# Kernel optimization log

Measured on AMD Instinct MI355X. Metric: run time of the kernel, lower is better.

## Reference

```python
import jax, jax.numpy as jnp
import numpy as np

IN_CH = 256
HID = 64
HEADS = 3 * 0 + 4  # num_heads


def setup_inputs() -> dict:
    key = jax.random.key(0)
    ks = jax.random.split(key, 5)
    B, C, H, W = 2, IN_CH, 64, 64
    x = jax.random.normal(ks[0], (B, C, H, W), dtype=jnp.float32)
    # per-head embed conv (kernel 1 -> stored as [heads, 3*HID, C]); kaiming fan_out-ish scale
    w_embed = jax.random.normal(ks[1], (HEADS, 3 * HID, C), dtype=jnp.float32) * np.float32(np.sqrt(2.0 / (3 * HID)))
    b_embed = jnp.zeros((HEADS, 3 * HID), dtype=jnp.float32)
    # output ConvTranspose2d(hidden*heads -> C, kernel 1): weight [hidden*heads, C]
    w_out = jax.random.normal(ks[2], (HEADS * HID, C), dtype=jnp.float32) * np.float32(np.sqrt(2.0 / C))
    b_out = jnp.zeros((C,), dtype=jnp.float32)
    return {"x": x, "w_embed": w_embed, "b_embed": b_embed, "w_out": w_out, "b_out": b_out}


def reference(x, w_embed, b_embed, w_out, b_out):
    B, C, H, W = x.shape
    N = H * W
    nH = w_embed.shape[0]
    D = w_embed.shape[1] // 3
    scale = D ** -0.5
    # 1x1 embed conv per head: [B, nH, 3D, N]
    xf = x.reshape(B, C, N)
    qkv = jnp.einsum('bcn,hdc->bhdn', xf, w_embed) + b_embed[None, :, :, None]
    q, k, v = jnp.split(qkv, 3, axis=2)  # each [B, nH, D, N]
    attn = jnp.einsum('bhci,bhcj->bhij', q, k) * scale  # [B, nH, N, N]
    attn = jax.nn.softmax(attn, axis=-1)
    y = jnp.einsum('bhij,bhcj->bhci', attn, v)  # [B, nH, D, N]
    y = y.reshape(B, nH * D, N)
    # output 1x1 transposed conv (kernel 1 == plain 1x1 projection)
    out = jnp.einsum('bkn,kc->bcn', y, w_out) + b_out[None, :, None]
    out = out.reshape(B, C, H, W)
    return out + x  # residual
```

## Files before the change

kernel.cpp:

```cpp
#include <hip/hip_runtime.h>
#include <hip/hip_bf16.h>

#define NH   4
#define D_   64
#define N_   4096
#define C_   256
#define ME   768
#define QSCALE 0.18033688f

typedef float    f32x4  __attribute__((ext_vector_type(4)));
typedef float    f32x16 __attribute__((ext_vector_type(16)));
typedef _Float16 f16x8  __attribute__((ext_vector_type(8)));
typedef _Float16 f16x4  __attribute__((ext_vector_type(4)));

__global__ __launch_bounds__(256) void prep_kernel(const float* __restrict__ x,
                                                   const float* __restrict__ w_out,
                                                   _Float16* __restrict__ xT,
                                                   _Float16* __restrict__ w_outT) {
    __shared__ float T[64][68];
    const int t = threadIdx.x, bx = blockIdx.x;
    if (bx < 512) {
        const int n0 = (bx & 63) * 64, c0 = ((bx >> 6) & 3) * 64, b = bx >> 8;
        const float* xp = x + ((size_t)b * C_ + c0) * N_ + n0;
        #pragma unroll
        for (int r = 0; r < 4; ++r) {
            int idx = r * 256 + t;
            int c = idx >> 4, ng = (idx & 15) * 4;
            *(f32x4*)&T[c][ng] = *(const f32x4*)(xp + (size_t)c * N_ + ng);
        }
        __syncthreads();
        _Float16* dp = xT + ((size_t)b * N_ + n0) * C_ + c0;
        #pragma unroll
        for (int r = 0; r < 2; ++r) {
            int idx = r * 256 + t;
            int n = idx >> 3, cg = (idx & 7) * 8;
            f16x8 v;
            #pragma unroll
            for (int j = 0; j < 8; ++j) v[j] = (_Float16)T[cg + j][n];
            *(f16x8*)(dp + (size_t)n * C_ + cg) = v;
        }
    } else {
        int tile = bx - 512;
        int tc = tile & 3, tk = tile >> 2;
        #pragma unroll
        for (int r = 0; r < 4; ++r) {
            int idx = r * 256 + t;
            int kl = idx >> 4, cl = (idx & 15) * 4;
            *(f32x4*)&T[kl][cl] = *(const f32x4*)(w_out + (size_t)(tk * 64 + kl) * C_ + tc * 64 + cl);
        }
        __syncthreads();
        #pragma unroll
        for (int r = 0; r < 2; ++r) {
            int idx = r * 256 + t;
            int cl = idx >> 3, kg = (idx & 7) * 8;
            f16x8 v;
            #pragma unroll
            for (int j = 0; j < 8; ++j) v[j] = (_Float16)T[kg + j][cl];
            *(f16x8*)(w_outT + (size_t)(tc * 64 + cl) * C_ + tk * 64 + kg) = v;
        }
    }
}

__global__ __launch_bounds__(256) void qkv_gemm(const _Float16* __restrict__ xT,
                                                const float* __restrict__ w_embed,
                                                const float* __restrict__ b_embed,
                                                _Float16* __restrict__ qT,
                                                _Float16* __restrict__ kT,
                                                _Float16* __restrict__ vB) {
    __shared__ __align__(16) union SM {
        struct { _Float16 A[64][40], X[64][40]; } s;
        float Os[64][68];
    } sm;
    const int n0 = blockIdx.x * 64, mt = blockIdx.y, b = blockIdx.z;
    const int m0 = mt * 64;
    const int t = threadIdx.x;
    const int lane = t & 63, w = t >> 6, quad = lane >> 4, l16 = lane & 15;
    const int srow = t >> 2, skoff = (t & 3) * 8;
    const int h = mt / 3, r3 = mt - h * 3;
    const float oscale = (r3 == 0) ? QSCALE : 1.0f;
    const float* ap = w_embed + (size_t)(m0 + srow) * C_ + skoff;
    const _Float16* xp = xT + ((size_t)b * N_ + n0 + srow) * C_ + skoff;
    f32x4 a0pre = *(const f32x4*)(ap);
    f32x4 a1pre = *(const f32x4*)(ap + 4);
    f16x8 xpre  = *(const f16x8*)(xp);
    f32x4 acc[4] = {};
    for (int k0 = 0; k0 < C_; k0 += 32) {
        __syncthreads();
        {
            f16x8 av = { (_Float16)a0pre[0], (_Float16)a0pre[1], (_Float16)a0pre[2], (_Float16)a0pre[3],
                         (_Float16)a1pre[0], (_Float16)a1pre[1], (_Float16)a1pre[2], (_Float16)a1pre[3] };
            *(f16x8*)&sm.s.A[srow][skoff] = av;
            *(f16x8*)&sm.s.X[srow][skoff] = xpre;
        }
        __syncthreads();
        if (k0 + 32 < C_) {
            a0pre = *(const f32x4*)(ap + k0 + 32);
            a1pre = *(const f32x4*)(ap + k0 + 36);
            xpre  = *(const f16x8*)(xp + k0 + 32);
        }
        f16x8 af = *(const f16x8*)&sm.s.A[w * 16 + l16][quad * 8];
        #pragma unroll
        for (int nb = 0; nb < 4; ++nb) {
            f16x8 bf = *(const f16x8*)&sm.s.X[nb * 16 + l16][quad * 8];
            acc[nb] = __builtin_amdgcn_mfma_f32_16x16x32_f16(af, bf, acc[nb], 0, 0, 0);
        }
    }
    float bias[4];
    #pragma unroll
    for (int rg = 0; rg < 4; ++rg) bias[rg] = b_embed[m0 + w * 16 + quad * 4 + rg];
    __syncthreads();
    #pragma unroll
    for (int nb = 0; nb < 4; ++nb)
        #pragma unroll
        for (int rg = 0; rg < 4; ++rg)
            sm.Os[w * 16 + quad * 4 + rg][nb * 16 + l16] = (acc[nb][rg] + bias[rg]) * oscale;
    __syncthreads();
    const int bh = b * NH + h;
    if (r3 < 2) {
        _Float16* dst = (r3 ? kT : qT) + ((size_t)bh * N_ + n0) * D_;
        #pragma unroll
        for (int r = 0; r < 2; ++r) {
            int idx = r * 256 + t;
            int n = idx >> 3, mg = (idx & 7) * 8;
            f16x8 v;
            #pragma unroll
            for (int j = 0; j < 8; ++j) v[j] = (_Float16)sm.Os[mg + j][n];
            *(f16x8*)(dst + (size_t)n * D_ + mg) = v;
        }
    } else {
        _Float16* dst = vB + (size_t)bh * D_ * N_ + n0;
        #pragma unroll
        for (int r = 0; r < 2; ++r) {
            int idx = r * 256 + t;
            int d = idx >> 3, ng = (idx & 7) * 8;
            f32x4 a = *(const f32x4*)&sm.Os[d][ng];
            f32x4 b2 = *(const f32x4*)&sm.Os[d][ng + 4];
            f16x8 v = { (_Float16)a[0], (_Float16)a[1], (_Float16)a[2], (_Float16)a[3],
                        (_Float16)b2[0], (_Float16)b2[1], (_Float16)b2[2], (_Float16)b2[3] };
            *(f16x8*)(dst + (size_t)d * N_ + ng) = v;
        }
    }
}

__global__ __launch_bounds__(256, 4) void attn_kernel(const _Float16* __restrict__ qT,
                                                      const _Float16* __restrict__ kT,
                                                      const _Float16* __restrict__ vB,
                                                      _Float16* __restrict__ opart,
                                                      float* __restrict__ mpart,
                                                      float* __restrict__ lpart,
                                                      int splog) {
    __shared__ __align__(16) union SM {
        struct { _Float16 K[64][76], V[64][76]; } s;
        _Float16 Os[128][76];
    } sm;
    const int t = threadIdx.x;
    const int nsp = 1 << splog;
    const int qt = blockIdx.x, h = blockIdx.y;
    const int b = blockIdx.z >> splog, s = blockIdx.z & (nsp - 1);
    const int bh = b * NH + h, sbh = s * 8 + bh;
    const _Float16* kp = kT + (size_t)bh * N_ * D_;
    const _Float16* vp = vB + (size_t)bh * D_ * N_;
    const int lane = t & 63, w = t >> 6, l32 = lane & 31, hl = lane >> 5;
    const int srow = t >> 3, scol = (t & 7) * 8;

    const _Float16* qp = qT + ((size_t)bh * N_ + qt * 128 + w * 32 + l32) * D_;
    f16x8 qf[4];
    #pragma unroll
    for (int kc = 0; kc < 4; ++kc) qf[kc] = *(const f16x8*)(qp + kc * 16 + hl * 8);

    f32x16 oacc0 = {}, oacc1 = {};
    float m_run = 0.f, l_run = 0.f;

    const int niter = 64 >> splog;
    const int jt_lo = s * niter, jt_hi = jt_lo + niter;
    f16x8 kpre[2], vpre[2];
    #pragma unroll
    for (int r = 0; r < 2; ++r) {
        int row = srow + r * 32;
        kpre[r] = *(const f16x8*)(kp + (size_t)(jt_lo * 64 + row) * D_ + scol);
        vpre[r] = *(const f16x8*)(vp + (size_t)row * N_ + jt_lo * 64 + scol);
    }

    for (int jt = jt_lo; jt < jt_hi; ++jt) {
        __syncthreads();
        #pragma unroll
        for (int r = 0; r < 2; ++r) {
            int row = srow + r * 32;
            *(f16x8*)&sm.s.K[row][scol] = kpre[r];
            *(f16x8*)&sm.s.V[row][scol] = vpre[r];
        }
        __syncthreads();
        if (jt + 1 < jt_hi) {
            #pragma unroll
            for (int r = 0; r < 2; ++r) {
                int row = srow + r * 32;
                kpre[r] = *(const f16x8*)(kp + (size_t)((jt + 1) * 64 + row) * D_ + scol);
                vpre[r] = *(const f16x8*)(vp + (size_t)row * N_ + (jt + 1) * 64 + scol);
            }
        }
        f32x16 sa0 = {}, sa1 = {};
        #pragma unroll
        for (int kc = 0; kc < 4; ++kc) {
            f16x8 kf0 = *(const f16x8*)&sm.s.K[l32][kc * 16 + hl * 8];
            sa0 = __builtin_amdgcn_mfma_f32_32x32x16_f16(kf0, qf[kc], sa0, 0, 0, 0);
            f16x8 kf1 = *(const f16x8*)&sm.s.K[32 + l32][kc * 16 + hl * 8];
            sa1 = __builtin_amdgcn_mfma_f32_32x32x16_f16(kf1, qf[kc], sa1, 0, 0, 0);
        }
        if (jt == jt_lo) {
            f32x16 mm;
            #pragma unroll
            for (int r = 0; r < 16; ++r) mm[r] = fmaxf(sa0[r], sa1[r]);
            f32x4 m4;
            #pragma unroll
            for (int r = 0; r < 4; ++r)
                m4[r] = fmaxf(fmaxf(mm[r], mm[r + 4]), fmaxf(mm[r + 8], mm[r + 12]));
            float mx = fmaxf(fmaxf(m4[0], m4[1]), fmaxf(m4[2], m4[3]));
            mx = fmaxf(mx, __shfl_xor(mx, 32));
            m_run = mx + 8.0f;
        }
        #pragma unroll
        for (int r = 0; r < 16; ++r) sa0[r] = __builtin_amdgcn_exp2f(sa0[r] - m_run);
        #pragma unroll
        for (int r = 0; r < 16; ++r) sa1[r] = __builtin_amdgcn_exp2f(sa1[r] - m_run);
        f32x16 sv = sa0 + sa1;
        f32x4 s4;
        #pragma unroll
        for (int r = 0; r < 4; ++r) s4[r] = (sv[r] + sv[r + 4]) + (sv[r + 8] + sv[r + 12]);
        float rs = (s4[0] + s4[1]) + (s4[2] + s4[3]);
        rs += __shfl_xor(rs, 32);
        l_run += rs;
        #pragma unroll
        for (int jb = 0; jb < 2; ++jb) {
            const f32x16& sa = jb ? sa1 : sa0;
            union BU { f16x4 v; int d[2]; } bf[4];
            #pragma unroll
            for (int q = 0; q < 8; ++q)
                bf[q >> 1].d[q & 1] =
                    __builtin_bit_cast(int, __builtin_amdgcn_cvt_pkrtz(sa[2 * q], sa[2 * q + 1]));
            #pragma unroll
            for (int c = 0; c < 4; ++c) {
                const int vcol = jb * 32 + c * 8 + hl * 4;
                f16x4 va = *(const f16x4*)&sm.s.V[l32][vcol];
                oacc0 = __builtin_amdgcn_mfma_f32_32x32x8f16(va, bf[c].v, oacc0, 0, 0, 0);
                f16x4 vb = *(const f16x4*)&sm.s.V[32 + l32][vcol];
                oacc1 = __builtin_amdgcn_mfma_f32_32x32x8f16(vb, bf[c].v, oacc1, 0, 0, 0);
            }
        }
    }
    float linv = 1.f / l_run;
    if (hl == 0) {
        mpart[(size_t)sbh * N_ + qt * 128 + w * 32 + l32] = m_run;
        lpart[(size_t)sbh * N_ + qt * 128 + w * 32 + l32] = l_run;
    }
    __syncthreads();
    #pragma unroll
    for (int db = 0; db < 2; ++db) {
        const f32x16& oc = db ? oacc1 : oacc0;
        #pragma unroll
        for (int rq = 0; rq < 4; ++rq) {
            f16x4 pv = { (_Float16)(oc[rq * 4 + 0] * linv), (_Float16)(oc[rq * 4 + 1] * linv),
                         (_Float16)(oc[rq * 4 + 2] * linv), (_Float16)(oc[rq * 4 + 3] * linv) };
            *(f16x4*)&sm.Os[w * 32 + l32][db * 32 + rq * 8 + hl * 4] = pv;
        }
    }
    __syncthreads();
    _Float16* op = opart + ((size_t)sbh * N_ + qt * 128) * D_;
    #pragma unroll
    for (int r = 0; r < 4; ++r) {
        int idx = r * 256 + t;
        int i = idx >> 3, ch = (idx & 7) * 8;
        *(f16x8*)(op + (size_t)i * D_ + ch) = *(const f16x8*)&sm.Os[i][ch];
    }
}

__global__ __launch_bounds__(256) void projc_gemm(const _Float16* __restrict__ opart,
                                                  const float* __restrict__ mpart,
                                                  const float* __restrict__ lpart,
                                                  const _Float16* __restrict__ w_outT,
                                                  const float* __restrict__ b_out,
                                                  const float* __restrict__ x,
                                                  float* __restrict__ out) {
    __shared__ __align__(16) union SMP {
        struct {
            _Float16 Y[64][264];
            union { float W[4][64][4]; _Float16 A[128][40]; } u;
        } p;
        float Os[128][68];
    } sm;
    const int nt = blockIdx.x, chh = blockIdx.y, b = blockIdx.z;
    const int n0 = nt * 64, c0 = chh * 128;
    const int t = threadIdx.x;
    const int lane = t & 63, w = t >> 6, quad = lane >> 4, l16 = lane & 15;

    {
        const int nl = t & 63, hh = t >> 6;
        const int bh = b * NH + hh;
        float mv[4], lv[4];
        #pragma unroll
        for (int sI = 0; sI < 4; ++sI) {
            mv[sI] = mpart[(size_t)(sI * 8 + bh) * N_ + n0 + nl];
            lv[sI] = lpart[(size_t)(sI * 8 + bh) * N_ + n0 + nl];
        }
        float M = fmaxf(fmaxf(mv[0], mv[1]), fmaxf(mv[2], mv[3]));
        float ws[4], sum = 0.f;
        #pragma unroll
        for (int sI = 0; sI < 4; ++sI) {
            ws[sI] = __builtin_amdgcn_exp2f(mv[sI] - M) * lv[sI];
            sum += ws[sI];
        }
        float inv = 1.f / sum;
        #pragma unroll
        for (int sI = 0; sI < 4; ++sI) sm.p.u.W[hh][nl][sI] = ws[sI] * inv;
    }
    __syncthreads();

    #pragma unroll
    for (int it = 0; it < 8; ++it) {
        int idx = it * 256 + t;
        int n = idx >> 5, kg = (idx & 31) * 8;
        int hh = kg >> 6, d0 = kg & 63;
        const int bh = b * NH + hh;
        const float* Wn = &sm.p.u.W[hh][n][0];
        float accf[8] = {};
        #pragma unroll
        for (int sI = 0; sI < 4; ++sI) {
            f16x8 ov = *(const f16x8*)(opart + ((size_t)(sI * 8 + bh) * N_ + n0 + n) * D_ + d0);
            float wsv = Wn[sI];
            #pragma unroll
            for (int j = 0; j < 8; ++j) accf[j] += wsv * (float)ov[j];
        }
        f16x8 yv;
        #pragma unroll
        for (int j = 0; j < 8; ++j) yv[j] = (_Float16)accf[j];
        *(f16x8*)&sm.p.Y[n][kg] = yv;
    }
    __syncthreads();

    const int srow = t >> 1, skoff = (t & 1) * 16;
    const _Float16* ap = w_outT + (size_t)(c0 + srow) * C_ + skoff;
    f16x8 apre0 = *(const f16x8*)(ap);
    f16x8 apre1 = *(const f16x8*)(ap + 8);
    f32x4 acc[2][4] = {};
    for (int k0 = 0; k0 < C_; k0 += 32) {
        __syncthreads();
        *(f16x8*)&sm.p.u.A[srow][skoff]     = apre0;
        *(f16x8*)&sm.p.u.A[srow][skoff + 8] = apre1;
        __syncthreads();
        if (k0 + 32 < C_) {
            apre0 = *(const f16x8*)(ap + k0 + 32);
            apre1 = *(const f16x8*)(ap + k0 + 40);
        }
        #pragma unroll
        for (int cb = 0; cb < 2; ++cb) {
            f16x8 af = *(const f16x8*)&sm.p.u.A[w * 32 + cb * 16 + l16][quad * 8];
            #pragma unroll
            for (int nb = 0; nb < 4; ++nb) {
                f16x8 bf = *(const f16x8*)&sm.p.Y[nb * 16 + l16][k0 + quad * 8];
                acc[cb][nb] = __builtin_amdgcn_mfma_f32_16x16x32_f16(af, bf, acc[cb][nb], 0, 0, 0);
            }
        }
    }
    float bias[2][4];
    #pragma unroll
    for (int cb = 0; cb < 2; ++cb)
        #pragma unroll
        for (int rg = 0; rg < 4; ++rg)
            bias[cb][rg] = b_out[c0 + w * 32 + cb * 16 + quad * 4 + rg];
    __syncthreads();
    #pragma unroll
    for (int cb = 0; cb < 2; ++cb)
        #pragma unroll
        for (int nb = 0; nb < 4; ++nb)
            #pragma unroll
            for (int rg = 0; rg < 4; ++rg)
                sm.Os[w * 32 + cb * 16 + quad * 4 + rg][nb * 16 + l16] =
                    acc[cb][nb][rg] + bias[cb][rg];
    __syncthreads();
    const float* xp = x + ((size_t)b * C_ + c0) * N_ + n0;
    float* op = out + ((size_t)b * C_ + c0) * N_ + n0;
    #pragma unroll
    for (int r = 0; r < 8; ++r) {
        int idx = r * 256 + t;
        int c = idx >> 4, ng = (idx & 15) * 4;
        f32x4 v  = *(const f32x4*)&sm.Os[c][ng];
        f32x4 xv = *(const f32x4*)(xp + (size_t)c * N_ + ng);
        f32x4 o  = { v[0] + xv[0], v[1] + xv[1], v[2] + xv[2], v[3] + xv[3] };
        *(f32x4*)(op + (size_t)c * N_ + ng) = o;
    }
}

extern "C" void kernel_launch(void* const* d_in, const int* in_sizes, int n_in,
                              void* d_out, int out_size, void* d_ws, size_t ws_size,
                              hipStream_t stream) {
    const float* x       = (const float*)d_in[0];
    const float* w_embed = (const float*)d_in[1];
    const float* b_embed = (const float*)d_in[2];
    const float* w_out   = (const float*)d_in[3];
    const float* b_out   = (const float*)d_in[4];
    float* out = (float*)d_out;

    const int splog = 2;

    _Float16* base   = (_Float16*)d_ws;
    _Float16* xT     = base;
    _Float16* w_outT = base + 2293760;
    _Float16* qT     = base + 2359296;
    _Float16* kT     = base + 4456448;
    _Float16* vB     = base + 6553600;
    _Float16* opart  = base + 8650752;
    float*    mpart  = (float*)(opart + (size_t)4 * 8 * N_ * D_);
    float*    lpart  = mpart + (size_t)4 * 8 * N_;

    prep_kernel<<<dim3(528, 1, 1), 256, 0, stream>>>(x, w_out, xT, w_outT);
    qkv_gemm   <<<dim3(64, 12, 2), 256, 0, stream>>>(xT, w_embed, b_embed, qT, kT, vB);
    attn_kernel<<<dim3(32, 4, 2 << splog), 256, 0, stream>>>(qT, kT, vB, opart, mpart, lpart, splog);
    projc_gemm <<<dim3(64, 2, 2),  256, 0, stream>>>(opart, mpart, lpart, w_outT, b_out, x, out);
}
```

Baseline: 145.1 us.

## Double-buffer K/V LDS tiles, use 32x32x16 MFMA for PV via permlane32 swap

Double-buffers the K and V shared-memory tiles so each iteration needs only one barrier instead of two. On targets with permlane32_swap, the P·V product is rebuilt to use the wider 32x32x16 f16 MFMA: packed probabilities are rearranged across half-waves so each instruction consumes 8-element fragments, halving the MFMA count for that stage. It also raises wave priority around the MFMA sections. The cost is double the LDS for K/V, which may lower occupancy at 4 blocks per CU, plus extra cross-lane permutes.

```diff
diff --git a/kernel.cpp b/kernel.cpp
--- a/kernel.cpp
+++ b/kernel.cpp
@@ -12,6 +12,13 @@
 typedef float    f32x16 __attribute__((ext_vector_type(16)));
 typedef _Float16 f16x8  __attribute__((ext_vector_type(8)));
 typedef _Float16 f16x4  __attribute__((ext_vector_type(4)));
+typedef unsigned int u32x2 __attribute__((ext_vector_type(2)));
+
+#if defined(__has_builtin)
+#if __has_builtin(__builtin_amdgcn_permlane32_swap)
+#define HAVE_PERMLANE32_SWAP 1
+#endif
+#endif
 
 __global__ __launch_bounds__(256) void prep_kernel(const float* __restrict__ x,
                                                    const float* __restrict__ w_out,
@@ -150,7 +157,7 @@
                                                       float* __restrict__ lpart,
                                                       int splog) {
     __shared__ __align__(16) union SM {
-        struct { _Float16 K[64][76], V[64][76]; } s;
+        struct { _Float16 K[2][64][76], V[2][64][76]; } s;
         _Float16 Os[128][76];
     } sm;
     const int t = threadIdx.x;
@@ -181,13 +188,13 @@
         vpre[r] = *(const f16x8*)(vp + (size_t)row * N_ + jt_lo * 64 + scol);
     }
 
-    for (int jt = jt_lo; jt < jt_hi; ++jt) {
-        __syncthreads();
+    int buf = 0;
+    for (int jt = jt_lo; jt < jt_hi; ++jt, buf ^= 1) {
         #pragma unroll
         for (int r = 0; r < 2; ++r) {
             int row = srow + r * 32;
-            *(f16x8*)&sm.s.K[row][scol] = kpre[r];
-            *(f16x8*)&sm.s.V[row][scol] = vpre[r];
+            *(f16x8*)&sm.s.K[buf][row][scol] = kpre[r];
+            *(f16x8*)&sm.s.V[buf][row][scol] = vpre[r];
         }
         __syncthreads();
         if (jt + 1 < jt_hi) {
@@ -199,13 +206,15 @@
             }
         }
         f32x16 sa0 = {}, sa1 = {};
+        __builtin_amdgcn_s_setprio(1);
         #pragma unroll
         for (int kc = 0; kc < 4; ++kc) {
-            f16x8 kf0 = *(const f16x8*)&sm.s.K[l32][kc * 16 + hl * 8];
+            f16x8 kf0 = *(const f16x8*)&sm.s.K[buf][l32][kc * 16 + hl * 8];
             sa0 = __builtin_amdgcn_mfma_f32_32x32x16_f16(kf0, qf[kc], sa0, 0, 0, 0);
-            f16x8 kf1 = *(const f16x8*)&sm.s.K[32 + l32][kc * 16 + hl * 8];
+            f16x8 kf1 = *(const f16x8*)&sm.s.K[buf][32 + l32][kc * 16 + hl * 8];
             sa1 = __builtin_amdgcn_mfma_f32_32x32x16_f16(kf1, qf[kc], sa1, 0, 0, 0);
         }
+        __builtin_amdgcn_s_setprio(0);
         if (jt == jt_lo) {
             f32x16 mm;
             #pragma unroll
@@ -229,6 +238,34 @@
         float rs = (s4[0] + s4[1]) + (s4[2] + s4[3]);
         rs += __shfl_xor(rs, 32);
         l_run += rs;
+#ifdef HAVE_PERMLANE32_SWAP
+        #pragma unroll
+        for (int jb = 0; jb < 2; ++jb) {
+            const f32x16& sa = jb ? sa1 : sa0;
+            #pragma unroll
+            for (int kk = 0; kk < 2; ++kk) {
+                unsigned int pa = __builtin_bit_cast(unsigned int,
+                    __builtin_amdgcn_cvt_pkrtz(sa[kk * 8 + 0], sa[kk * 8 + 1]));
+                unsigned int pb = __builtin_bit_cast(unsigned int,
+                    __builtin_amdgcn_cvt_pkrtz(sa[kk * 8 + 2], sa[kk * 8 + 3]));
+                unsigned int pc = __builtin_bit_cast(unsigned int,
+                    __builtin_amdgcn_cvt_pkrtz(sa[kk * 8 + 4], sa[kk * 8 + 5]));
+                unsigned int pd = __builtin_bit_cast(unsigned int,
+                    __builtin_amdgcn_cvt_pkrtz(sa[kk * 8 + 6], sa[kk * 8 + 7]));
+                u32x2 r0 = __builtin_amdgcn_permlane32_swap(pa, pc, false, false);
+                u32x2 r1 = __builtin_amdgcn_permlane32_swap(pb, pd, false, false);
+                union PF { unsigned int u[4]; f16x8 v; } pf;
+                pf.u[0] = r0[0]; pf.u[1] = r1[0]; pf.u[2] = r0[1]; pf.u[3] = r1[1];
+                const int vcol = jb * 32 + kk * 16 + hl * 8;
+                f16x8 va  = *(const f16x8*)&sm.s.V[buf][l32][vcol];
+                f16x8 vb2 = *(const f16x8*)&sm.s.V[buf][32 + l32][vcol];
+                __builtin_amdgcn_s_setprio(1);
+                oacc0 = __builtin_amdgcn_mfma_f32_32x32x16_f16(va, pf.v, oacc0, 0, 0, 0);
+                oacc1 = __builtin_amdgcn_mfma_f32_32x32x16_f16(vb2, pf.v, oacc1, 0, 0, 0);
+                __builtin_amdgcn_s_setprio(0);
+            }
+        }
+#else
         #pragma unroll
         for (int jb = 0; jb < 2; ++jb) {
             const f32x16& sa = jb ? sa1 : sa0;
@@ -240,12 +277,13 @@
             #pragma unroll
             for (int c = 0; c < 4; ++c) {
                 const int vcol = jb * 32 + c * 8 + hl * 4;
-                f16x4 va = *(const f16x4*)&sm.s.V[l32][vcol];
+                f16x4 va = *(const f16x4*)&sm.s.V[buf][l32][vcol];
                 oacc0 = __builtin_amdgcn_mfma_f32_32x32x8f16(va, bf[c].v, oacc0, 0, 0, 0);
-                f16x4 vb = *(const f16x4*)&sm.s.V[32 + l32][vcol];
+                f16x4 vb = *(const f16x4*)&sm.s.V[buf][32 + l32][vcol];
                 oacc1 = __builtin_amdgcn_mfma_f32_32x32x8f16(vb, bf[c].v, oacc1, 0, 0, 0);
             }
         }
+#endif
     }
     float linv = 1.f / l_run;
     if (hl == 0) {
```

New measurement: 149.2 us. 1.03x slower.
